# Kernel optimization log

Measured on AMD Instinct MI355X. Metric: run time of the kernel, lower is better.

## Reference

```python
import jax, jax.numpy as jnp
import numpy as np
import math

K, N, T, HID = 10, 96, 40, 48   # samples, agents (batch_size=1), timesteps, hidden
HZ = 10.0
R0, R1 = 0.5, 4.0
SPB = 6                          # social pooling grid is 6x6
RSTEP = (R1 - R0) / SPB          # radius_step (not set in shown source; natural value)
TWO_PI = 2.0 * math.pi
TSTEP = TWO_PI / SPB             # theta_step


def setup_inputs() -> dict:
    key = jax.random.key(0)
    ks = iter(jax.random.split(key, 24))
    def u(shape, fan):
        s = 1.0 / float(np.sqrt(fan))
        return jax.random.uniform(next(ks), shape, jnp.float32, -s, s)
    inp = {
        "hx": jax.random.normal(next(ks), (N, HID), jnp.float32),
        # locations in [-15,15] keep feature-map pixel gather in-bounds (u=40-long(y))
        "current_location": (jax.random.uniform(next(ks), (N, 2), jnp.float32) - 0.5) * 30.0,
        "y_path": (jax.random.uniform(next(ks), (K, T, N, 2), jnp.float32) - 0.5) * 30.0,
        "image_data": jax.random.normal(next(ks), (1, 4, 160, 160), jnp.float32),
        "conv1_w": u((16, 4, 5, 5), 4 * 25), "conv1_b": u((16,), 4 * 25),
        "conv2_w": u((32, 16, 5, 5), 16 * 25), "conv2_b": u((32,), 16 * 25),
        "fcvel_w": u((16, 2), 2), "fcvel_b": u((16,), 2),
        "gru_wih": u((3 * HID, 96), 96), "gru_whh": u((3 * HID, HID), HID),
        "gru_bih": u((3 * HID,), HID), "gru_bhh": u((3 * HID,), HID),
        "fcscf_w": u((HID, SPB * SPB * HID), SPB * SPB * HID), "fcscf_b": u((HID,), SPB * SPB * HID),
        "fcscore_w": u((1, HID), HID), "fcscore_b": u((1,), HID),
        "fcdy_w": u((2 * T, HID), HID), "fcdy_b": u((2 * T,), HID),
    }
    return inp


def _forward(hx, current_location, y_path, image_data, conv1_w, conv1_b, conv2_w, conv2_b,
             fcvel_w, fcvel_b, gru_wih, gru_whh, gru_bih, gru_bhh,
             fcscf_w, fcscf_b, fcscore_w, fcscore_b, fcdy_w, fcdy_b):
    # cnn_map: (1,4,160,160) -> (1,32,80,80)
    x = jax.lax.conv_general_dilated(image_data, conv1_w, (2, 2), ((2, 2), (2, 2)),
                                     dimension_numbers=("NCHW", "OIHW", "NCHW"))
    x = jax.nn.relu(x + conv1_b[None, :, None, None])
    x = jax.lax.conv_general_dilated(x, conv2_w, (1, 1), ((2, 2), (2, 2)),
                                     dimension_numbers=("NCHW", "OIHW", "NCHW"))
    fmap = jax.nn.relu(x + conv2_b[None, :, None, None])[0]  # (32,80,80); batch_size=1
    H = fmap.shape[1]

    # compute_vel + fc_vel: (K,T,N,2) -> (K,T,N,16)
    prev = jnp.concatenate([jnp.broadcast_to(current_location[None, None], (K, 1, N, 2)),
                            y_path[:, :-1]], axis=1)
    vel = (y_path - prev) * HZ
    y_fv = jax.nn.relu(vel @ fcvel_w.T + fcvel_b)

    hx_all = jnp.tile(hx, (K, 1))  # hx.repeat((K,1)) -> (K*N,48)
    t_idx = jnp.arange(N)
    not_self = ~jnp.eye(N, dtype=bool)

    def step(h, xs):
        loc, fv_t = xs  # (K,N,2), (K,N,16)
        hidden = h[:N]  # replicates hx[0:n] slice used in the original scf call
        # feature-map gather at agent pixel (.long() truncates toward zero)
        ui = (H // 2) - loc[..., 1].astype(jnp.int32)
        vi = (H // 2) - loc[..., 0].astype(jnp.int32)
        feat = jnp.moveaxis(fmap[:, ui, vi], 0, -1)  # (K,N,32)
        # pairwise dist/angle binning: c[k,j,t] = loc_t - loc_j
        c = loc[:, None, :, :] - loc[:, :, None, :]
        dist = jnp.linalg.norm(c, axis=-1)                        # (K,N,N)
        valid = (dist >= R0) & (dist <= R1) & not_self[None]
        dsafe = jnp.maximum(dist, 1e-10)
        cost = jnp.clip(c[..., 0] / dsafe, -1.0, 1.0)
        ac = jnp.arccos(cost)
        theta = jnp.where(c[..., 1] < 0, TWO_PI - ac, ac)
        ub = jnp.clip(((dist - R0) / RSTEP).astype(jnp.int32), 0, SPB - 1)
        vb = jnp.clip((theta / TSTEP).astype(jnp.int32), 0, SPB - 1)
        bins = ub * SPB + vb                                      # (K,N,N)
        hot = (bins[..., None] == jnp.arange(SPB * SPB)) & valid[..., None]  # (K,N,N,36)
        counts = hot.sum(axis=2)                                  # (K,N,36)
        # original writes hidden[t] with set() in increasing-t order: last writer = max t
        winner = jnp.max(jnp.where(hot, t_idx[None, None, :, None], -1), axis=2)
        sp = jnp.where(winner[..., None] >= 0, hidden[jnp.maximum(winner, 0)], 0.0)  # (K,N,36,48)
        sp = sp / jnp.maximum(counts, 1)[..., None]
        sps = sp.reshape(K, N, SPB * SPB * HID)
        lhalf = jnp.concatenate([feat, fv_t], axis=-1)            # (K,N,48)
        rhalf = jax.nn.relu(sps @ fcscf_w.T + fcscf_b)            # (K,N,48)
        x_i = jnp.concatenate([lhalf, rhalf], axis=-1).reshape(K * N, 96)
        # torch GRUCell (gate order r,z,n)
        gi = x_i @ gru_wih.T + gru_bih
        gh = h @ gru_whh.T + gru_bhh
        ir, iz, inn = jnp.split(gi, 3, axis=-1)
        hr, hz_, hn = jnp.split(gh, 3, axis=-1)
        r = jax.nn.sigmoid(ir + hr)
        z = jax.nn.sigmoid(iz + hz_)
        ng = jnp.tanh(inn + r * hn)
        h_new = (1.0 - z) * ng + z * h
        return h_new, h_new

    xs = (jnp.moveaxis(y_path, 1, 0), jnp.moveaxis(y_fv, 1, 0))  # time-major
    h_last, hs = jax.lax.scan(step, hx_all, xs)                  # hs: (T,K*N,48)
    delta_y = jax.nn.relu(h_last @ fcdy_w.T + fcdy_b)            # (K*N,80)
    delta_y = delta_y.reshape(K, N, 2, T).transpose(0, 3, 1, 2)  # (K,40,N,2)
    score = (hs @ fcscore_w.T + fcscore_b).sum(axis=0).reshape(K, N, 1)
    return delta_y, score


def reference(hx, current_location, y_path, image_data, conv1_w, conv1_b, conv2_w, conv2_b,
              fcvel_w, fcvel_b, gru_wih, gru_whh, gru_bih, gru_bhh,
              fcscf_w, fcscf_b, fcscore_w, fcscore_b, fcdy_w, fcdy_b):
    return _forward(hx, current_location, y_path, image_data, conv1_w, conv1_b, conv2_w, conv2_b,
                    fcvel_w, fcvel_b, gru_wih, gru_whh, gru_bih, gru_bhh,
                    fcscf_w, fcscf_b, fcscore_w, fcscore_b, fcdy_w, fcdy_b)
```

## Files before the change

kernel.cpp:

```cpp
#include <hip/hip_runtime.h>
#include <math.h>

#define KK 10
#define NN 96
#define TT 40

#define HZf 10.0f
#define R0f 0.5f
#define R1f 4.0f
#define RSTEPf ((4.0f - 0.5f) / 6.0f)
#define TWO_PIf 6.2831853071795864769f
#define TSTEPf (6.2831853071795864769f / 6.0f)

typedef unsigned short u16;
typedef unsigned int u32;
typedef unsigned long long u64;
typedef float f32x4 __attribute__((ext_vector_type(4)));

__device__ __forceinline__ u16 f2bf(float f) {
    union { float f; unsigned u; } v; v.f = f;
    unsigned r = v.u + 0x7fffu + ((v.u >> 16) & 1u);
    return (u16)(r >> 16);
}
__device__ __forceinline__ float bflo(u32 u) {
// ... 16 lines not shown
    const int tid = threadIdx.x;
    const int bx = blockIdx.x % 10, by = blockIdx.x / 10;
    const int x0 = bx * 8, y0 = by * 8;
    for (int i = tid; i < 1600; i += 256) {
        int oc = i & 15, t2 = i >> 4, tap = t2 % 25, ic = t2 / 25;
        sW[i] = w[(oc * 4 + ic) * 25 + tap];
    }
    for (int i = tid; i < 1444; i += 256) {
        int ic = i / 361, rem = i % 361, r = rem / 19, c = rem % 19;
        int gy = 2 * y0 - 2 + r, gx = 2 * x0 - 2 + c;
        sIn[i] = (gy >= 0 && gy < 160 && gx >= 0 && gx < 160)
                     ? img[(ic * 160 + gy) * 160 + gx] : 0.f;
    }
    __syncthreads();
    const int pix = tid & 63, ocg = tid >> 6;
    const int px = pix & 7, py = pix >> 3;
    float acc[4];
#pragma unroll
    for (int j = 0; j < 4; ++j) acc[j] = b[ocg * 4 + j];
#pragma unroll
    for (int ic = 0; ic < 4; ++ic) {
        int ibase = ic * 361;
#pragma unroll
        for (int ky = 0; ky < 5; ++ky) {
#pragma unroll
            for (int kx = 0; kx < 5; ++kx) {
                float iv = sIn[ibase + (2 * py + ky) * 19 + 2 * px + kx];
                f32x4 wv = *(const f32x4*)&sW[(ic * 25 + ky * 5 + kx) * 16 + ocg * 4];
#pragma unroll
                for (int j = 0; j < 4; ++j) acc[j] += iv * wv[j];
            }
        }
    }
#pragma unroll
    for (int j = 0; j < 4; ++j)
        out[((ocg * 4 + j) * 80 + y0 + py) * 80 + x0 + px] = fmaxf(acc[j], 0.f);
}

__global__ __launch_bounds__(256) void conv2_t(const float* __restrict__ in,
                                               const float* __restrict__ w,
                                               const float* __restrict__ b,
                                               float* __restrict__ out) {
    __shared__ float sW[12800];
    __shared__ float sIn[2304];
    const int tid = threadIdx.x;
    const int bx = blockIdx.x % 10, by = blockIdx.x / 10;
    const int x0 = bx * 8, y0 = by * 8;
    for (int i = tid; i < 12800; i += 256) {
        int oc = i & 31, t2 = i >> 5, tap = t2 % 25, ic = t2 / 25;
        sW[i] = w[(oc * 16 + ic) * 25 + tap];
    }
    for (int i = tid; i < 2304; i += 256) {
        int ic = i / 144, rem = i % 144, r = rem / 12, c = rem % 12;
        int gy = y0 - 2 + r, gx = x0 - 2 + c;
        sIn[i] = (gy >= 0 && gy < 80 && gx >= 0 && gx < 80)
                     ? in[(ic * 80 + gy) * 80 + gx] : 0.f;
    }
    __syncthreads();
    const int pix = tid & 63, ocg = tid >> 6;
    const int px = pix & 7, py = pix >> 3;
    float acc[8];
#pragma unroll
    for (int j = 0; j < 8; ++j) acc[j] = b[ocg * 8 + j];
    for (int ic = 0; ic < 16; ++ic) {
        int ibase = ic * 144;
#pragma unroll
        for (int ky = 0; ky < 5; ++ky) {
#pragma unroll
            for (int kx = 0; kx < 5; ++kx) {
                float iv = sIn[ibase + (py + ky) * 12 + px + kx];
                int wb = (ic * 25 + ky * 5 + kx) * 32 + ocg * 8;
                f32x4 w0 = *(const f32x4*)&sW[wb];
                f32x4 w1 = *(const f32x4*)&sW[wb + 4];
#pragma unroll
                for (int j = 0; j < 4; ++j) {
                    acc[j] += iv * w0[j];
                    acc[4 + j] += iv * w1[j];
                }
            }
        }
    }
#pragma unroll
    for (int j = 0; j < 8; ++j)
        out[((ocg * 8 + j) * 80 + y0 + py) * 80 + x0 + px] = fmaxf(acc[j], 0.f);
}

__global__ void prep_w3(const float* __restrict__ scf, const float* __restrict__ wih,
                        const float* __restrict__ whh, const float* __restrict__ bih,
                        const float* __restrict__ bhh, const float* __restrict__ scfb,
                        const float* __restrict__ hx, float* __restrict__ h0hist,
                        u32* __restrict__ wscf_p, u32* __restrict__ Wr_p,
                        u32* __restrict__ Wz_p, u32* __restrict__ Win_p,
                        u32* __restrict__ Whn_p, float* __restrict__ bias5) {
    int idx = blockIdx.x * blockDim.x + threadIdx.x;
    if (idx < 41472) {
        int o = idx % 48, dp = (idx / 48) % 24, b = idx / 1152;
        float v0 = scf[o * 1728 + b * 48 + 2 * dp];
        float v1 = scf[o * 1728 + b * 48 + 2 * dp + 1];
        wscf_p[idx] = (u32)f2bf(v0) | ((u32)f2bf(v1) << 16);
    } else if (idx < 44928) {
        int j = idx - 41472, od = j % 48, dp = j / 48;
        int kk0 = 2 * dp, kk1 = 2 * dp + 1;
        float v0 = kk0 < 96 ? wih[od * 96 + kk0] : whh[od * 48 + kk0 - 96];
        float v1 = kk1 < 96 ? wih[od * 96 + kk1] : whh[od * 48 + kk1 - 96];
        Wr_p[j] = (u32)f2bf(v0) | ((u32)f2bf(v1) << 16);
    } else if (idx < 48384) {
        int j = idx - 44928, od = j % 48, dp = j / 48;
        int row = 48 + od, kk0 = 2 * dp, kk1 = 2 * dp + 1;
        float v0 = kk0 < 96 ? wih[row * 96 + kk0] : whh[row * 48 + kk0 - 96];
        float v1 = kk1 < 96 ? wih[row * 96 + kk1] : whh[row * 48 + kk1 - 96];
        Wz_p[j] = (u32)f2bf(v0) | ((u32)f2bf(v1) << 16);
    } else if (idx < 50688) {
        int j = idx - 48384, od = j % 48, dp = j / 48;
        int row = 96 + od;
        Win_p[j] = (u32)f2bf(wih[row * 96 + 2 * dp]) | ((u32)f2bf(wih[row * 96 + 2 * dp + 1]) << 16);
    } else if (idx < 51840) {
        int j = idx - 50688, od = j % 48, dp = j / 48;
        int row = 96 + od;
        Whn_p[j] = (u32)f2bf(whh[row * 48 + 2 * dp]) | ((u32)f2bf(whh[row * 48 + 2 * dp + 1]) << 16);
    } else if (idx < 52080) {
        int j = idx - 51840, od = j % 48, q = j / 48;
        float v;
        if (q == 0) v = bih[od] + bhh[od];
        else if (q == 1) v = bih[48 + od] + bhh[48 + od];
        else if (q == 2) v = bih[96 + od];
        else if (q == 3) v = bhh[96 + od];
        else v = scfb[od];
        bias5[j] = v;
    } else if (idx < 56688) {
        int j = idx - 52080;
        h0hist[j] = hx[j];
    }
}

__global__ __launch_bounds__(256) void lhalf_k(const float* __restrict__ yp,
                                               const float* __restrict__ cur,
                                               const float* __restrict__ fmap,
                                               const float* __restrict__ vw,
                                               const float* __restrict__ vb,
                                               u16* __restrict__ lhalf_bf) {
    int item = blockIdx.x * 4 + (threadIdx.x >> 6);
    int lane = threadIdx.x & 63;
    int n = item % NN, k = (item / NN) % KK, t = item / (KK * NN);
    float lx = yp[((k * TT + t) * NN + n) * 2 + 0];
    float ly = yp[((k * TT + t) * NN + n) * 2 + 1];
    float px, py;
    if (t == 0) { px = cur[n * 2]; py = cur[n * 2 + 1]; }
    else { px = yp[((k * TT + t - 1) * NN + n) * 2]; py = yp[((k * TT + t - 1) * NN + n) * 2 + 1]; }
    float vx = (lx - px) * HZf, vy = (ly - py) * HZf;
    int ui = 40 - (int)ly;
    int vi = 40 - (int)lx;
    ui = min(max(ui, 0), 79);
    vi = min(max(vi, 0), 79);
    int row = k * NN + n;
    u16* dst = lhalf_bf + ((size_t)t * 960 + row) * 48;
    if (lane < 32) {
        dst[lane] = f2bf(fmap[(lane * 80 + ui) * 80 + vi]);
    } else if (lane < 48) {
        int f = lane - 32;
        float a = vb[f] + vx * vw[f * 2 + 0] + vy * vw[f * 2 + 1];
        dst[lane] = f2bf(fmaxf(a, 0.0f));
    }
}

__global__ __launch_bounds__(256) void bins4_k(const float* __restrict__ yp,
                                               u32* __restrict__ binc) {
    int tk = blockIdx.x;
    int k = tk % KK, t = tk / KK;
    int tid = threadIdx.x;
    __shared__ float xs[96], ys[96];
    __shared__ int win_s[96 * 36];
    __shared__ int cnt_s[96 * 36];
    if (tid < 96) {
        xs[tid] = yp[((k * TT + t) * NN + tid) * 2 + 0];
        ys[tid] = yp[((k * TT + t) * NN + tid) * 2 + 1];
    }
    for (int i = tid; i < 96 * 36; i += 256) { win_s[i] = -1; cnt_s[i] = 0; }
    __syncthreads();
    for (int p = tid; p < 96 * 96; p += 256) {
        int i = p / 96, j = p % 96;
        if (i == j) continue;
        float dx = xs[j] - xs[i], dy = ys[j] - ys[i];
        float dist = sqrtf(dx * dx + dy * dy);
        if (dist < R0f || dist > R1f) continue;
        float dsafe = fmaxf(dist, 1e-10f);
        float cost = fminf(fmaxf(dx / dsafe, -1.0f), 1.0f);
        float ac = acosf(cost);
        float theta = (dy < 0.0f) ? (TWO_PIf - ac) : ac;
        int ub = (int)((dist - R0f) / RSTEPf); ub = min(max(ub, 0), 5);
        int vb = (int)(theta / TSTEPf);        vb = min(max(vb, 0), 5);
        int b = ub * 6 + vb;
        atomicAdd(&cnt_s[i * 36 + b], 1);
        atomicMax(&win_s[i * 36 + b], j);
    }
    __syncthreads();
    if (tid < 96) {
        u32 base = (u32)(t * 960 + k * 96 + tid) * 20u;
        u16* entg = (u16*)(binc + base + 2);
        u64 mask = 0ull;
        int ne = 0;
        for (int b = 0; b < 36; ++b) {
            int w = win_s[tid * 36 + b];
            if (w >= 0) {
                mask |= 1ull << b;
                entg[ne++] = (u16)((w << 8) | cnt_s[tid * 36 + b]);
            }
        }
        binc[base] = (u32)mask;
        binc[base + 1] = (u32)(mask >> 32);
    }
}

__global__ __launch_bounds__(256) void step_k(
    int t, float* __restrict__ h0hist, const u16* __restrict__ lhalf_bf,
    const u32* __restrict__ binc, const u32* __restrict__ wscf_p,
    const u32* __restrict__ Wr_p, const u32* __restrict__ Wz_p,
    const u32* __restrict__ Win_p, const u32* __restrict__ Whn_p,
    const float* __restrict__ bias5, const float* __restrict__ scw,
    float* __restrict__ score_acc, float* __restrict__ hfin,
    u16* __restrict__ rhalf_all, const float* __restrict__ hx,
    float* __restrict__ hf) {
    __shared__ u32 smu[9856];
    float* smf = (float*)smu;
    const int tid = threadIdx.x;
    const int wv = tid >> 6, lane = tid & 63;
    const int lo = lane < 48 ? lane : 47;

    if (blockIdx.x < 96) {
        if (t >= TT) return;
        const float* hcur = h0hist + (size_t)t * 4608;
        const int r = blockIdx.x;
        float* shw = smf;
        float* shx = smf + 1728;
        float* ps1 = smf + 1872;
        float* ps2 = smf + 2064;
        u32* sent = (u32*)(smf + 2832);
        unsigned char* blist = (unsigned char*)(smf + 2852);

        if (tid < 20) sent[tid] = binc[(size_t)(t * 960 + r) * 20 + tid];
        if (tid < 48) {
            shx[tid] = bf2f(lhalf_bf[((size_t)t * 960 + r) * 48 + tid]);
            shx[96 + tid] = hcur[r * 48 + tid];
        }
        __syncthreads();
        u64 mask = ((u64)sent[1] << 32) | sent[0];
        int ne = __popcll(mask);
        const u16* ent = (const u16*)(sent + 2);
        if (tid < 36 && ((mask >> tid) & 1)) {
            int rank = __popcll(mask & ((1ull << tid) - 1ull));
            blist[rank] = (unsigned char)tid;
        }
        for (int i = tid; i < ne * 48; i += 256) {
            int e = i / 48, c = i - e * 48;
            int w = (ent[e] >> 8) & 0xff;
            shw[i] = hcur[w * 48 + c];
        }
        __syncthreads();
        float acc = 0.f;
        for (int e = 0; e < ne; ++e) {
            int b = blist[e];
            float cinv = 1.0f / (float)(ent[e] & 0xff);
            const u32* wp = wscf_p + (b * 24 + wv * 6) * 48 + lo;
            const float* xv = shw + e * 48 + wv * 12;
            float a = 0.f;
#pragma unroll
            for (int dp = 0; dp < 6; ++dp) {
                u32 u = wp[dp * 48];
                a += bflo(u) * xv[2 * dp] + bfhi(u) * xv[2 * dp + 1];
            }
            acc += a * cinv;
        }
        if (lane < 48) ps1[wv * 48 + lane] = acc;
        __syncthreads();
        if (wv == 0 && lane < 48) {
            float rh = ps1[lane] + ps1[48 + lane] + ps1[96 + lane] + ps1[144 + lane] +
                       bias5[192 + lane];
            shx[48 + lane] = fmaxf(rh, 0.f);
        }
        __syncthreads();
        float aR = 0.f, aZ = 0.f, aI = 0.f, aH = 0.f;
        int dp0 = wv * 18;
#pragma unroll
        for (int i = 0; i < 18; ++i) {
            int dp = dp0 + i;
            u32 uR = Wr_p[dp * 48 + lo], uZ = Wz_p[dp * 48 + lo];
            float xlo = shx[2 * dp], xhi = shx[2 * dp + 1];
            aR += bflo(uR) * xlo + bfhi(uR) * xhi;
            aZ += bflo(uZ) * xlo + bfhi(uZ) * xhi;
            if (dp < 48) {
                u32 uI = Win_p[dp * 48 + lo];
                aI += bflo(uI) * xlo + bfhi(uI) * xhi;
            } else {
                u32 uH = Whn_p[(dp - 48) * 48 + lo];
                aH += bflo(uH) * xlo + bfhi(uH) * xhi;
            }
        }
        if (lane < 48) {
            ps2[(wv * 4 + 0) * 48 + lane] = aR;
            ps2[(wv * 4 + 1) * 48 + lane] = aZ;
            ps2[(wv * 4 + 2) * 48 + lane] = aI;
            ps2[(wv * 4 + 3) * 48 + lane] = aH;
        }
        __syncthreads();
        if (wv == 0) {
            float sv = 0.f;
            if (lane < 48) {
                float AR = 0.f, AZ = 0.f, AI = 0.f, AH = 0.f;
#pragma unroll
                for (int w2 = 0; w2 < 4; ++w2) {
                    AR += ps2[(w2 * 4 + 0) * 48 + lane];
                    AZ += ps2[(w2 * 4 + 1) * 48 + lane];
                    AI += ps2[(w2 * 4 + 2) * 48 + lane];
                    AH += ps2[(w2 * 4 + 3) * 48 + lane];
                }
                float hprev = shx[96 + lane];
                float rr = sigmoidf_(AR + bias5[lane]);
                float zz = sigmoidf_(AZ + bias5[48 + lane]);
                float ng = tanhf(AI + bias5[96 + lane] + rr * (AH + bias5[144 + lane]));
                float hn = (1.0f - zz) * ng + zz * hprev;
                h0hist[(size_t)(t + 1) * 4608 + r * 48 + lane] = hn;
                if (t == TT - 1) hfin[r * 48 + lane] = hn;
                sv = hn * scw[lane];
            }
            for (int off = 32; off; off >>= 1) sv += __shfl_down(sv, off);
            if (lane == 0) score_acc[r] = (t == 0 ? 0.f : score_acc[r]) + sv;
        }
    } else if (blockIdx.x < 312) {
        if (t >= TT) return;
        const float* hcur = h0hist + (size_t)t * 4608;
        int widx = (blockIdx.x - 96) * 4 + wv;
        int row = 96 + widx;
        float* myw = smf + wv * 1728;
        const u32* bp = binc + (size_t)(t * 960 + row) * 20;
        u64 mask = ((u64)bp[1] << 32) | bp[0];
        int ne = __popcll(mask);
        const u16* ent = (const u16*)(bp + 2);
        for (int i = lane; i < ne * 48; i += 64) {
            int e = i / 48, c = i - e * 48;
            int w = (ent[e] >> 8) & 0xff;
            myw[i] = hcur[w * 48 + c];
        }
        __syncthreads();
        float acc = 0.f;
        u64 m2 = mask;
        for (int e = 0; e < ne; ++e) {
            int b = __ffsll((long long)m2) - 1;
            m2 &= m2 - 1;
            float cinv = 1.0f / (float)(ent[e] & 0xff);
            const u32* wp = wscf_p + b * 24 * 48 + lo;
            const float* xv = myw + e * 48;
            float a = 0.f;
#pragma unroll 8
            for (int dp = 0; dp < 24; ++dp) {
                u32 u = wp[dp * 48];
                a += bflo(u) * xv[2 * dp] + bfhi(u) * xv[2 * dp + 1];
            }
            acc += a * cinv;
        }
        float rh = fmaxf(acc + bias5[192 + lo], 0.f);
        if (lane < 48) rhalf_all[((size_t)t * 864 + widx) * 48 + lane] = f2bf(rh);
    } else {
        int s = t - 1;
        if (s < 0 || s >= TT) return;
        u32* sWr = smu;
        u32* sWz = smu + 3456;
        u32* sWin = smu + 6912;
        u32* sx = smu + 9216 + wv * 48;
        float* shh = (float*)(smu + 9408) + wv * 48;
        for (int i = tid; i < 3456; i += 256) { sWr[i] = Wr_p[i]; sWz[i] = Wz_p[i]; }
        for (int i = tid; i < 2304; i += 256) sWin[i] = Win_p[i];
        u32 whn[24];
#pragma unroll
        for (int dp = 0; dp < 24; ++dp) whn[dp] = Whn_p[dp * 48 + lo];
        int widx = (blockIdx.x - 312) * 4 + wv;
        int row = 96 + widx;
        const float* hsrc = (s == 0) ? (hx + (row % 96) * 48) : (hf + (s & 1) * 41472 + widx * 48);
        float hreg = hsrc[lo];
        if (lane < 24) {
            sx[lane] = *(const u32*)(lhalf_bf + ((size_t)s * 960 + row) * 48 + 2 * lane);
            sx[24 + lane] = *(const u32*)(rhalf_all + ((size_t)s * 864 + widx) * 48 + 2 * lane);
        }
        if (lane < 48) shh[lane] = hreg;
        __syncthreads();
        const float bRb = bias5[lo], bZb = bias5[48 + lo], bIb = bias5[96 + lo],
                    bHb = bias5[144 + lo];
        float aR = 0.f, aZ = 0.f, aI = 0.f, aH = 0.f;
#pragma unroll 8
        for (int dp = 0; dp < 48; ++dp) {
            u32 xp = sx[dp];
            float xlo = bflo(xp), xhi = bfhi(xp);
            u32 uR = sWr[dp * 48 + lo], uZ = sWz[dp * 48 + lo], uI = sWin[dp * 48 + lo];
            aR += bflo(uR) * xlo + bfhi(uR) * xhi;
            aZ += bflo(uZ) * xlo + bfhi(uZ) * xhi;
            aI += bflo(uI) * xlo + bfhi(uI) * xhi;
        }
#pragma unroll 8
        for (int dp = 48; dp < 72; ++dp) {
            float xlo = shh[2 * dp - 96], xhi = shh[2 * dp - 95];
            u32 uR = sWr[dp * 48 + lo], uZ = sWz[dp * 48 + lo], uH = whn[dp - 48];
            aR += bflo(uR) * xlo + bfhi(uR) * xhi;
            aZ += bflo(uZ) * xlo + bfhi(uZ) * xhi;
            aH += bflo(uH) * xlo + bfhi(uH) * xhi;
        }
        float rr = sigmoidf_(aR + bRb);
        float zz = sigmoidf_(aZ + bZb);
        float ng = tanhf(aI + bIb + rr * (aH + bHb));
        float hn = (1.0f - zz) * ng + zz * hreg;
        if (lane < 48) {
            hf[((s + 1) & 1) * 41472 + widx * 48 + lane] = hn;
            if (s == TT - 1) hfin[(size_t)row * 48 + lane] = hn;
        }
        float sv = (lane < 48) ? hn * scw[lane] : 0.f;
        for (int off = 32; off; off >>= 1) sv += __shfl_down(sv, off);
        if (lane == 0) score_acc[row] = (s == 0 ? 0.f : score_acc[row]) + sv;
    }
}

__global__ void final_k(const float* __restrict__ hlast, const float* __restrict__ score_acc,
                        const float* __restrict__ dyw, const float* __restrict__ dyb,
                        const float* __restrict__ scoreb, float* __restrict__ out) {
    int row = blockIdx.x, lane = threadIdx.x;
    int n = row % 96, k = row / 96;
    __shared__ float sh_h[48];
    if (lane < 48) sh_h[lane] = hlast[row * 48 + lane];
    __syncthreads();
    if (lane < 80) {
        float a = dyb[lane];
#pragma unroll 8
        for (int d = 0; d < 48; d++) a += sh_h[d] * dyw[lane * 48 + d];
        a = fmaxf(a, 0.0f);
        int j = lane / 40, tt = lane % 40;
        out[((k * TT + tt) * NN + n) * 2 + j] = a;
    } else if (lane == 80) {
        out[76800 + row] = score_acc[row] + 40.0f * scoreb[0];
    }
}

// ... 3 lines not shown
    const float* hx  = (const float*)d_in[0];
    const float* cur = (const float*)d_in[1];
    const float* yp  = (const float*)d_in[2];
    const float* img = (const float*)d_in[3];
    const float* c1w = (const float*)d_in[4];
    const float* c1b = (const float*)d_in[5];
    const float* c2w = (const float*)d_in[6];
    const float* c2b = (const float*)d_in[7];
    const float* vw  = (const float*)d_in[8];
    const float* vb  = (const float*)d_in[9];
    const float* wih = (const float*)d_in[10];
    const float* whh = (const float*)d_in[11];
    const float* bih = (const float*)d_in[12];
    const float* bhh = (const float*)d_in[13];
    const float* scfw = (const float*)d_in[14];
    const float* scfb = (const float*)d_in[15];
    const float* scw  = (const float*)d_in[16];
    const float* scb  = (const float*)d_in[17];
    const float* dyw  = (const float*)d_in[18];
    const float* dyb  = (const float*)d_in[19];
    float* out = (float*)d_out;

    char* ws = (char*)d_ws;
    u32*   binc     = (u32*)(ws + 0);
    float* fmap1    = (float*)(ws + 0);
    float* fmap     = (float*)(ws + 409600);
    u16*   rhalf_all= (u16*)(ws + 3072000);
    u16*   lhalf_bf = (u16*)(ws + 6389760);
    float* h0hist   = (float*)(ws + 10076160);
    float* hfin     = (float*)(ws + 10831872);
    float* score_acc= (float*)(ws + 11016192);
    u32*   wscf_p   = (u32*)(ws + 11020032);
    u32*   Wr_p     = (u32*)(ws + 11185920);
    u32*   Wz_p     = (u32*)(ws + 11199744);
    u32*   Win_p    = (u32*)(ws + 11213568);
    u32*   Whn_p    = (u32*)(ws + 11222784);
    float* bias5    = (float*)(ws + 11227392);
    float* hf       = (float*)(ws + 11228352);

    conv1_t<<<100, 256, 0, stream>>>(img, c1w, c1b, fmap1);
    conv2_t<<<100, 256, 0, stream>>>(fmap1, c2w, c2b, fmap);
    prep_w3<<<222, 256, 0, stream>>>(scfw, wih, whh, bih, bhh, scfb, hx, h0hist,
                                     wscf_p, Wr_p, Wz_p, Win_p, Whn_p, bias5);
    lhalf_k<<<TT * KK * NN / 4, 256, 0, stream>>>(yp, cur, fmap, vw, vb, lhalf_bf);
    bins4_k<<<TT * KK, 256, 0, stream>>>(yp, binc);

    for (int t = 0; t <= TT; ++t) {
        step_k<<<528, 256, 0, stream>>>(t, h0hist, lhalf_bf, binc, wscf_p, Wr_p, Wz_p,
                                        Win_p, Whn_p, bias5, scw, score_acc, hfin,
                                        rhalf_all, hx, hf);
    }
    final_k<<<960, 128, 0, stream>>>(hfin, score_acc, dyw, dyb, scb, out);
}
```

Before: 490.1 us.

## Fuse preprocessing kernels and advance two GRU timesteps per launch

Merges the weight-packing, lhalf and social-bin kernels into one launch. The recurrent step kernel now processes two timesteps per launch, with agent blocks recomputing the needed neighbour rows for the intermediate step, which halves the number of serialized step launches. The cost is redundant per-block recomputation of dependent rows and more shared memory and register pressure in the step kernel. The workspace layout is also moved so that binc no longer aliases fmap1.

After: 1.467 ms. 199% more time.

```diff
diff --git a/kernel.cpp b/kernel.cpp
--- a/kernel.cpp
+++ b/kernel.cpp
@@ -62,7 +62,7 @@
     for (int ic = 0; ic < 4; ++ic) {
         int ibase = ic * 361;
 #pragma unroll
-        for (int ky = 0; ky < 5; ++ky) {
+        for (int ky = 0; ky < 5; ++ky)
 #pragma unroll
             for (int kx = 0; kx < 5; ++kx) {
                 float iv = sIn[ibase + (2 * py + ky) * 19 + 2 * px + kx];
@@ -70,7 +70,6 @@
 #pragma unroll
                 for (int j = 0; j < 4; ++j) acc[j] += iv * wv[j];
             }
-        }
     }
 #pragma unroll
     for (int j = 0; j < 4; ++j)
@@ -105,7 +104,7 @@
     for (int ic = 0; ic < 16; ++ic) {
         int ibase = ic * 144;
 #pragma unroll
-        for (int ky = 0; ky < 5; ++ky) {
+        for (int ky = 0; ky < 5; ++ky)
 #pragma unroll
             for (int kx = 0; kx < 5; ++kx) {
                 float iv = sIn[ibase + (py + ky) * 12 + px + kx];
@@ -113,145 +112,207 @@
                 f32x4 w0 = *(const f32x4*)&sW[wb];
                 f32x4 w1 = *(const f32x4*)&sW[wb + 4];
 #pragma unroll
-                for (int j = 0; j < 4; ++j) {
-                    acc[j] += iv * w0[j];
-                    acc[4 + j] += iv * w1[j];
-                }
-            }
-        }
+                for (int j = 0; j < 4; ++j) { acc[j] += iv * w0[j]; acc[4 + j] += iv * w1[j]; }
+            }
     }
 #pragma unroll
     for (int j = 0; j < 8; ++j)
         out[((ocg * 8 + j) * 80 + y0 + py) * 80 + x0 + px] = fmaxf(acc[j], 0.f);
 }
 
-__global__ void prep_w3(const float* __restrict__ scf, const float* __restrict__ wih,
-                        const float* __restrict__ whh, const float* __restrict__ bih,
-                        const float* __restrict__ bhh, const float* __restrict__ scfb,
-                        const float* __restrict__ hx, float* __restrict__ h0hist,
-                        u32* __restrict__ wscf_p, u32* __restrict__ Wr_p,
-                        u32* __restrict__ Wz_p, u32* __restrict__ Win_p,
-                        u32* __restrict__ Whn_p, float* __restrict__ bias5) {
-    int idx = blockIdx.x * blockDim.x + threadIdx.x;
-    if (idx < 41472) {
-        int o = idx % 48, dp = (idx / 48) % 24, b = idx / 1152;
-        float v0 = scf[o * 1728 + b * 48 + 2 * dp];
-        float v1 = scf[o * 1728 + b * 48 + 2 * dp + 1];
-        wscf_p[idx] = (u32)f2bf(v0) | ((u32)f2bf(v1) << 16);
-    } else if (idx < 44928) {
-        int j = idx - 41472, od = j % 48, dp = j / 48;
-        int kk0 = 2 * dp, kk1 = 2 * dp + 1;
-        float v0 = kk0 < 96 ? wih[od * 96 + kk0] : whh[od * 48 + kk0 - 96];
-        float v1 = kk1 < 96 ? wih[od * 96 + kk1] : whh[od * 48 + kk1 - 96];
-        Wr_p[j] = (u32)f2bf(v0) | ((u32)f2bf(v1) << 16);
-    } else if (idx < 48384) {
-        int j = idx - 44928, od = j % 48, dp = j / 48;
-        int row = 48 + od, kk0 = 2 * dp, kk1 = 2 * dp + 1;
-        float v0 = kk0 < 96 ? wih[row * 96 + kk0] : whh[row * 48 + kk0 - 96];
-        float v1 = kk1 < 96 ? wih[row * 96 + kk1] : whh[row * 48 + kk1 - 96];
-        Wz_p[j] = (u32)f2bf(v0) | ((u32)f2bf(v1) << 16);
-    } else if (idx < 50688) {
-        int j = idx - 48384, od = j % 48, dp = j / 48;
-        int row = 96 + od;
-        Win_p[j] = (u32)f2bf(wih[row * 96 + 2 * dp]) | ((u32)f2bf(wih[row * 96 + 2 * dp + 1]) << 16);
-    } else if (idx < 51840) {
-        int j = idx - 50688, od = j % 48, dp = j / 48;
-        int row = 96 + od;
-        Whn_p[j] = (u32)f2bf(whh[row * 48 + 2 * dp]) | ((u32)f2bf(whh[row * 48 + 2 * dp + 1]) << 16);
-    } else if (idx < 52080) {
-        int j = idx - 51840, od = j % 48, q = j / 48;
-        float v;
-        if (q == 0) v = bih[od] + bhh[od];
-        else if (q == 1) v = bih[48 + od] + bhh[48 + od];
-        else if (q == 2) v = bih[96 + od];
-        else if (q == 3) v = bhh[96 + od];
-        else v = scfb[od];
-        bias5[j] = v;
-    } else if (idx < 56688) {
-        int j = idx - 52080;
-        h0hist[j] = hx[j];
-    }
-}
-
-__global__ __launch_bounds__(256) void lhalf_k(const float* __restrict__ yp,
-                                               const float* __restrict__ cur,
-                                               const float* __restrict__ fmap,
-                                               const float* __restrict__ vw,
-                                               const float* __restrict__ vb,
-                                               u16* __restrict__ lhalf_bf) {
-    int item = blockIdx.x * 4 + (threadIdx.x >> 6);
-    int lane = threadIdx.x & 63;
-    int n = item % NN, k = (item / NN) % KK, t = item / (KK * NN);
-    float lx = yp[((k * TT + t) * NN + n) * 2 + 0];
-    float ly = yp[((k * TT + t) * NN + n) * 2 + 1];
-    float px, py;
-    if (t == 0) { px = cur[n * 2]; py = cur[n * 2 + 1]; }
-    else { px = yp[((k * TT + t - 1) * NN + n) * 2]; py = yp[((k * TT + t - 1) * NN + n) * 2 + 1]; }
-    float vx = (lx - px) * HZf, vy = (ly - py) * HZf;
-    int ui = 40 - (int)ly;
-    int vi = 40 - (int)lx;
-    ui = min(max(ui, 0), 79);
-    vi = min(max(vi, 0), 79);
-    int row = k * NN + n;
-    u16* dst = lhalf_bf + ((size_t)t * 960 + row) * 48;
-    if (lane < 32) {
-        dst[lane] = f2bf(fmap[(lane * 80 + ui) * 80 + vi]);
-    } else if (lane < 48) {
-        int f = lane - 32;
-        float a = vb[f] + vx * vw[f * 2 + 0] + vy * vw[f * 2 + 1];
-        dst[lane] = f2bf(fmaxf(a, 0.0f));
-    }
-}
-
-__global__ __launch_bounds__(256) void bins4_k(const float* __restrict__ yp,
-                                               u32* __restrict__ binc) {
-    int tk = blockIdx.x;
-    int k = tk % KK, t = tk / KK;
-    int tid = threadIdx.x;
+__global__ __launch_bounds__(256) void pre_k(
+    const float* __restrict__ scf, const float* __restrict__ wih,
+    const float* __restrict__ whh, const float* __restrict__ bih,
+    const float* __restrict__ bhh, const float* __restrict__ scfb,
+    const float* __restrict__ hx, float* __restrict__ h0hist,
+    u32* __restrict__ wscf_p, u32* __restrict__ Wr_p, u32* __restrict__ Wz_p,
+    u32* __restrict__ Win_p, u32* __restrict__ Whn_p, float* __restrict__ bias5,
+    const float* __restrict__ yp, const float* __restrict__ cur,
+    const float* __restrict__ fmap, const float* __restrict__ vw,
+    const float* __restrict__ vb, u16* __restrict__ lhalf_bf,
+    u32* __restrict__ binc) {
     __shared__ float xs[96], ys[96];
     __shared__ int win_s[96 * 36];
     __shared__ int cnt_s[96 * 36];
-    if (tid < 96) {
-        xs[tid] = yp[((k * TT + t) * NN + tid) * 2 + 0];
-        ys[tid] = yp[((k * TT + t) * NN + tid) * 2 + 1];
-    }
-    for (int i = tid; i < 96 * 36; i += 256) { win_s[i] = -1; cnt_s[i] = 0; }
-    __syncthreads();
-    for (int p = tid; p < 96 * 96; p += 256) {
-        int i = p / 96, j = p % 96;
-        if (i == j) continue;
-        float dx = xs[j] - xs[i], dy = ys[j] - ys[i];
-        float dist = sqrtf(dx * dx + dy * dy);
-        if (dist < R0f || dist > R1f) continue;
-        float dsafe = fmaxf(dist, 1e-10f);
-        float cost = fminf(fmaxf(dx / dsafe, -1.0f), 1.0f);
-        float ac = acosf(cost);
-        float theta = (dy < 0.0f) ? (TWO_PIf - ac) : ac;
-        int ub = (int)((dist - R0f) / RSTEPf); ub = min(max(ub, 0), 5);
-        int vb = (int)(theta / TSTEPf);        vb = min(max(vb, 0), 5);
-        int b = ub * 6 + vb;
-        atomicAdd(&cnt_s[i * 36 + b], 1);
-        atomicMax(&win_s[i * 36 + b], j);
-    }
-    __syncthreads();
-    if (tid < 96) {
-        u32 base = (u32)(t * 960 + k * 96 + tid) * 20u;
-        u16* entg = (u16*)(binc + base + 2);
-        u64 mask = 0ull;
-        int ne = 0;
-        for (int b = 0; b < 36; ++b) {
-            int w = win_s[tid * 36 + b];
-            if (w >= 0) {
-                mask |= 1ull << b;
-                entg[ne++] = (u16)((w << 8) | cnt_s[tid * 36 + b]);
-            }
-        }
-        binc[base] = (u32)mask;
-        binc[base + 1] = (u32)(mask >> 32);
-    }
-}
-
-__global__ __launch_bounds__(256) void step_k(
+    const int bid = blockIdx.x;
+    if (bid < 222) {
+        int idx = bid * 256 + threadIdx.x;
+        if (idx < 41472) {
+            int o = idx % 48, dp = (idx / 48) % 24, b = idx / 1152;
+            float v0 = scf[o * 1728 + b * 48 + 2 * dp];
+            float v1 = scf[o * 1728 + b * 48 + 2 * dp + 1];
+            wscf_p[idx] = (u32)f2bf(v0) | ((u32)f2bf(v1) << 16);
+        } else if (idx < 44928) {
+            int j = idx - 41472, od = j % 48, dp = j / 48;
+            int kk0 = 2 * dp, kk1 = 2 * dp + 1;
+            float v0 = kk0 < 96 ? wih[od * 96 + kk0] : whh[od * 48 + kk0 - 96];
+            float v1 = kk1 < 96 ? wih[od * 96 + kk1] : whh[od * 48 + kk1 - 96];
+            Wr_p[j] = (u32)f2bf(v0) | ((u32)f2bf(v1) << 16);
+        } else if (idx < 48384) {
+            int j = idx - 44928, od = j % 48, dp = j / 48;
+            int row = 48 + od, kk0 = 2 * dp, kk1 = 2 * dp + 1;
+            float v0 = kk0 < 96 ? wih[row * 96 + kk0] : whh[row * 48 + kk0 - 96];
+            float v1 = kk1 < 96 ? wih[row * 96 + kk1] : whh[row * 48 + kk1 - 96];
+            Wz_p[j] = (u32)f2bf(v0) | ((u32)f2bf(v1) << 16);
+        } else if (idx < 50688) {
+            int j = idx - 48384, od = j % 48, dp = j / 48;
+            int row = 96 + od;
+            Win_p[j] = (u32)f2bf(wih[row * 96 + 2 * dp]) |
+                       ((u32)f2bf(wih[row * 96 + 2 * dp + 1]) << 16);
+        } else if (idx < 51840) {
+            int j = idx - 50688, od = j % 48, dp = j / 48;
+            int row = 96 + od;
+            Whn_p[j] = (u32)f2bf(whh[row * 48 + 2 * dp]) |
+                       ((u32)f2bf(whh[row * 48 + 2 * dp + 1]) << 16);
+        } else if (idx < 52080) {
+            int j = idx - 51840, od = j % 48, q = j / 48;
+            float v;
+            if (q == 0) v = bih[od] + bhh[od];
+            else if (q == 1) v = bih[48 + od] + bhh[48 + od];
+            else if (q == 2) v = bih[96 + od];
+            else if (q == 3) v = bhh[96 + od];
+            else v = scfb[od];
+            bias5[j] = v;
+        } else if (idx < 56688) {
+            int j = idx - 52080;
+            h0hist[j] = hx[j];
+        }
+    } else if (bid < 222 + 9600) {
+        int item = (bid - 222) * 4 + (threadIdx.x >> 6);
+        int lane = threadIdx.x & 63;
+        int n = item % NN, k = (item / NN) % KK, t = item / (KK * NN);
+        float lx = yp[((k * TT + t) * NN + n) * 2 + 0];
+        float ly = yp[((k * TT + t) * NN + n) * 2 + 1];
+        float px, py;
+        if (t == 0) { px = cur[n * 2]; py = cur[n * 2 + 1]; }
+        else { px = yp[((k * TT + t - 1) * NN + n) * 2]; py = yp[((k * TT + t - 1) * NN + n) * 2 + 1]; }
+        float vx = (lx - px) * HZf, vy = (ly - py) * HZf;
+        int ui = 40 - (int)ly, vi = 40 - (int)lx;
+        ui = min(max(ui, 0), 79);
+        vi = min(max(vi, 0), 79);
+        int row = k * NN + n;
+        u16* dst = lhalf_bf + ((size_t)t * 960 + row) * 48;
+        if (lane < 32) {
+            dst[lane] = f2bf(fmap[(lane * 80 + ui) * 80 + vi]);
+        } else if (lane < 48) {
+            int f = lane - 32;
+            float a = vb[f] + vx * vw[f * 2 + 0] + vy * vw[f * 2 + 1];
+            dst[lane] = f2bf(fmaxf(a, 0.0f));
+        }
+    } else {
+        int tk = bid - 222 - 9600;
+        int k = tk % KK, t = tk / KK;
+        int tid = threadIdx.x;
+        if (tid < 96) {
+            xs[tid] = yp[((k * TT + t) * NN + tid) * 2 + 0];
+            ys[tid] = yp[((k * TT + t) * NN + tid) * 2 + 1];
+        }
+        for (int i = tid; i < 96 * 36; i += 256) { win_s[i] = -1; cnt_s[i] = 0; }
+        __syncthreads();
+        for (int p = tid; p < 96 * 96; p += 256) {
+            int i = p / 96, j = p % 96;
+            if (i == j) continue;
+            float dx = xs[j] - xs[i], dy = ys[j] - ys[i];
+            float dist = sqrtf(dx * dx + dy * dy);
+            if (dist < R0f || dist > R1f) continue;
+            float dsafe = fmaxf(dist, 1e-10f);
+            float cost = fminf(fmaxf(dx / dsafe, -1.0f), 1.0f);
+            float ac = acosf(cost);
+            float theta = (dy < 0.0f) ? (TWO_PIf - ac) : ac;
+            int ub = (int)((dist - R0f) / RSTEPf); ub = min(max(ub, 0), 5);
+            int vb = (int)(theta / TSTEPf);        vb = min(max(vb, 0), 5);
+            int b = ub * 6 + vb;
+            atomicAdd(&cnt_s[i * 36 + b], 1);
+            atomicMax(&win_s[i * 36 + b], j);
+        }
+        __syncthreads();
+        if (tid < 96) {
+            u32 base = (u32)(t * 960 + k * 96 + tid) * 20u;
+            u16* entg = (u16*)(binc + base + 2);
+            u64 mask = 0ull;
+            int ne = 0;
+            for (int b = 0; b < 36; ++b) {
+                int w = win_s[tid * 36 + b];
+                if (w >= 0) {
+                    mask |= 1ull << b;
+                    entg[ne++] = (u16)((w << 8) | cnt_s[tid * 36 + b]);
+                }
+            }
+            binc[base] = (u32)mask;
+            binc[base + 1] = (u32)(mask >> 32);
+        }
+    }
+}
+
+__device__ __forceinline__ float rhalf_row(const u32* __restrict__ bp,
+                                           const float* __restrict__ hsrc,
+                                           const u32* __restrict__ wscf_p, int lo,
+                                           const float* __restrict__ biasL) {
+    u64 mask = ((u64)bp[1] << 32) | (u64)bp[0];
+    int ne = __popcll(mask);
+    const u16* ent = (const u16*)(bp + 2);
+    float acc = 0.f;
+    u64 m2 = mask;
+    for (int e = 0; e < ne; ++e) {
+        int b = __ffsll((long long)m2) - 1;
+        m2 &= m2 - 1;
+        u32 en = ent[e];
+        int win = (en >> 8) & 0xff;
+        float cinv = 1.f / (float)(en & 0xff);
+        const u32* wp = wscf_p + (b * 24) * 48 + lo;
+        const float* xv = hsrc + win * 48;
+        float a = 0.f;
+#pragma unroll 8
+        for (int dp = 0; dp < 24; ++dp) {
+            u32 u = wp[dp * 48];
+            a += bflo(u) * xv[2 * dp] + bfhi(u) * xv[2 * dp + 1];
+        }
+        acc += a * cinv;
+    }
+    return fmaxf(acc + biasL[192 + lo], 0.f);
+}
+
+__device__ __forceinline__ float stepA_row(
+    int w, int t, int lo, const float* __restrict__ hT, const u16* __restrict__ lhT,
+    const u32* __restrict__ binc, const u32* __restrict__ wscf_p,
+    const u32* __restrict__ Wr_p, const u32* __restrict__ Wz_p,
+    const u32* __restrict__ Win_p, const u32* __restrict__ Whn_p,
+    const float* __restrict__ biasL) {
+    const u32* bp = binc + (size_t)(t * 960 + w) * 20;
+    float rh = rhalf_row(bp, hT, wscf_p, lo, biasL);
+    float aR = 0.f, aZ = 0.f, aI = 0.f, aH = 0.f;
+#pragma unroll 8
+    for (int dp = 0; dp < 24; ++dp) {
+        u32 xp = *(const u32*)&lhT[w * 48 + 2 * dp];
+        float xlo = bflo(xp), xhi = bfhi(xp);
+        u32 uR = Wr_p[dp * 48 + lo], uZ = Wz_p[dp * 48 + lo], uI = Win_p[dp * 48 + lo];
+        aR += bflo(uR) * xlo + bfhi(uR) * xhi;
+        aZ += bflo(uZ) * xlo + bfhi(uZ) * xhi;
+        aI += bflo(uI) * xlo + bfhi(uI) * xhi;
+    }
+#pragma unroll 8
+    for (int dp = 24; dp < 48; ++dp) {
+        float xlo = __shfl(rh, 2 * dp - 48), xhi = __shfl(rh, 2 * dp - 47);
+        u32 uR = Wr_p[dp * 48 + lo], uZ = Wz_p[dp * 48 + lo], uI = Win_p[dp * 48 + lo];
+        aR += bflo(uR) * xlo + bfhi(uR) * xhi;
+        aZ += bflo(uZ) * xlo + bfhi(uZ) * xhi;
+        aI += bflo(uI) * xlo + bfhi(uI) * xhi;
+    }
+#pragma unroll 8
+    for (int dp = 48; dp < 72; ++dp) {
+        float xlo = hT[w * 48 + 2 * dp - 96], xhi = hT[w * 48 + 2 * dp - 95];
+        u32 uR = Wr_p[dp * 48 + lo], uZ = Wz_p[dp * 48 + lo], uH = Whn_p[(dp - 48) * 48 + lo];
+        aR += bflo(uR) * xlo + bfhi(uR) * xhi;
+        aZ += bflo(uZ) * xlo + bfhi(uZ) * xhi;
+        aH += bflo(uH) * xlo + bfhi(uH) * xhi;
+    }
+    float rr = sigmoidf_(aR + biasL[lo]);
+    float zz = sigmoidf_(aZ + biasL[48 + lo]);
+    float ng = tanhf(aI + biasL[96 + lo] + rr * (aH + biasL[144 + lo]));
+    return (1.f - zz) * ng + zz * hT[w * 48 + lo];
+}
+
+__global__ __launch_bounds__(256) void step2_k(
     int t, float* __restrict__ h0hist, const u16* __restrict__ lhalf_bf,
     const u32* __restrict__ binc, const u32* __restrict__ wscf_p,
     const u32* __restrict__ Wr_p, const u32* __restrict__ Wz_p,
@@ -260,48 +321,64 @@
     float* __restrict__ score_acc, float* __restrict__ hfin,
     u16* __restrict__ rhalf_all, const float* __restrict__ hx,
     float* __restrict__ hf) {
-    __shared__ u32 smu[9856];
-    float* smf = (float*)smu;
+    __shared__ char smem[52000];
     const int tid = threadIdx.x;
     const int wv = tid >> 6, lane = tid & 63;
     const int lo = lane < 48 ? lane : 47;
-
-    if (blockIdx.x < 96) {
+    const int bid = blockIdx.x;
+
+    if (bid < 96) {
         if (t >= TT) return;
-        const float* hcur = h0hist + (size_t)t * 4608;
-        const int r = blockIdx.x;
-        float* shw = smf;
-        float* shx = smf + 1728;
-        float* ps1 = smf + 1872;
-        float* ps2 = smf + 2064;
-        u32* sent = (u32*)(smf + 2832);
-        unsigned char* blist = (unsigned char*)(smf + 2852);
-
-        if (tid < 20) sent[tid] = binc[(size_t)(t * 960 + r) * 20 + tid];
+        float* hT = (float*)smem;
+        float* h1 = (float*)(smem + 18432);
+        u16* lhT = (u16*)(smem + 36864);
+        float* biasL = (float*)(smem + 46080);
+        float* scwL = (float*)(smem + 47040);
+        u32* sentB = (u32*)(smem + 47232);
+        float* shxB = (float*)(smem + 47312);
+        float* ps1 = (float*)(smem + 47888);
+        float* ps2 = (float*)(smem + 48656);
+        const int r = bid;
+        for (int i = tid; i < 4608; i += 256) hT[i] = h0hist[(size_t)t * 4608 + i];
+        {
+            const u32* src = (const u32*)(lhalf_bf + (size_t)t * 960 * 48);
+            for (int i = tid; i < 2304; i += 256) ((u32*)lhT)[i] = src[i];
+        }
+        if (tid < 240) biasL[tid] = bias5[tid];
+        if (tid < 48) scwL[tid] = scw[tid];
+        if (tid < 20) sentB[tid] = binc[(size_t)((t + 1) * 960 + r) * 20 + tid];
+        __syncthreads();
+        u64 maskB = ((u64)sentB[1] << 32) | (u64)sentB[0];
+        int neB = __popcll(maskB);
+        const u16* entB = (const u16*)(sentB + 2);
+        int nS = neB + 1;
+        float scoreA = 0.f;
+        for (int idx = wv; idx < nS; idx += 4) {
+            int w = (idx == 0) ? r : ((entB[idx - 1] >> 8) & 0xff);
+            float hn = stepA_row(w, t, lo, hT, lhT, binc, wscf_p, Wr_p, Wz_p, Win_p,
+                                 Whn_p, biasL);
+            if (lane < 48) h1[w * 48 + lane] = hn;
+            if (idx == 0) {
+                scoreA = (lane < 48) ? hn * scwL[lane] : 0.f;
+                if (lane < 48) h0hist[(size_t)(t + 1) * 4608 + r * 48 + lane] = hn;
+            }
+        }
+        __syncthreads();
         if (tid < 48) {
-            shx[tid] = bf2f(lhalf_bf[((size_t)t * 960 + r) * 48 + tid]);
-            shx[96 + tid] = hcur[r * 48 + tid];
-        }
-        __syncthreads();
-        u64 mask = ((u64)sent[1] << 32) | sent[0];
-        int ne = __popcll(mask);
-        const u16* ent = (const u16*)(sent + 2);
-        if (tid < 36 && ((mask >> tid) & 1)) {
-            int rank = __popcll(mask & ((1ull << tid) - 1ull));
-            blist[rank] = (unsigned char)tid;
-        }
-        for (int i = tid; i < ne * 48; i += 256) {
-            int e = i / 48, c = i - e * 48;
-            int w = (ent[e] >> 8) & 0xff;
-            shw[i] = hcur[w * 48 + c];
+            shxB[tid] = bf2f(lhalf_bf[((size_t)(t + 1) * 960 + r) * 48 + tid]);
+            shxB[96 + tid] = h1[r * 48 + tid];
         }
         __syncthreads();
         float acc = 0.f;
-        for (int e = 0; e < ne; ++e) {
-            int b = blist[e];
-            float cinv = 1.0f / (float)(ent[e] & 0xff);
+        u64 m2 = maskB;
+        for (int e = 0; e < neB; ++e) {
+            int b = __ffsll((long long)m2) - 1;
+            m2 &= m2 - 1;
+            u32 en = entB[e];
+            int win = (en >> 8) & 0xff;
+            float cinv = 1.f / (float)(en & 0xff);
             const u32* wp = wscf_p + (b * 24 + wv * 6) * 48 + lo;
-            const float* xv = shw + e * 48 + wv * 12;
+            const float* xv = h1 + win * 48 + wv * 12;
             float a = 0.f;
 #pragma unroll
             for (int dp = 0; dp < 6; ++dp) {
@@ -314,8 +391,8 @@
         __syncthreads();
         if (wv == 0 && lane < 48) {
             float rh = ps1[lane] + ps1[48 + lane] + ps1[96 + lane] + ps1[144 + lane] +
-                       bias5[192 + lane];
-            shx[48 + lane] = fmaxf(rh, 0.f);
+                       biasL[192 + lane];
+            shxB[48 + lane] = fmaxf(rh, 0.f);
         }
         __syncthreads();
         float aR = 0.f, aZ = 0.f, aI = 0.f, aH = 0.f;
@@ -324,7 +401,7 @@
         for (int i = 0; i < 18; ++i) {
             int dp = dp0 + i;
             u32 uR = Wr_p[dp * 48 + lo], uZ = Wz_p[dp * 48 + lo];
-            float xlo = shx[2 * dp], xhi = shx[2 * dp + 1];
+            float xlo = shxB[2 * dp], xhi = shxB[2 * dp + 1];
             aR += bflo(uR) * xlo + bfhi(uR) * xhi;
             aZ += bflo(uZ) * xlo + bfhi(uZ) * xhi;
             if (dp < 48) {
@@ -343,7 +420,7 @@
         }
         __syncthreads();
         if (wv == 0) {
-            float sv = 0.f;
+            float sv = scoreA;
             if (lane < 48) {
                 float AR = 0.f, AZ = 0.f, AI = 0.f, AH = 0.f;
 #pragma unroll
@@ -353,106 +430,134 @@
                     AI += ps2[(w2 * 4 + 2) * 48 + lane];
                     AH += ps2[(w2 * 4 + 3) * 48 + lane];
                 }
-                float hprev = shx[96 + lane];
-                float rr = sigmoidf_(AR + bias5[lane]);
-                float zz = sigmoidf_(AZ + bias5[48 + lane]);
-                float ng = tanhf(AI + bias5[96 + lane] + rr * (AH + bias5[144 + lane]));
+                float hprev = shxB[96 + lane];
+                float rr = sigmoidf_(AR + biasL[lane]);
+                float zz = sigmoidf_(AZ + biasL[48 + lane]);
+                float ng = tanhf(AI + biasL[96 + lane] + rr * (AH + biasL[144 + lane]));
                 float hn = (1.0f - zz) * ng + zz * hprev;
-                h0hist[(size_t)(t + 1) * 4608 + r * 48 + lane] = hn;
-                if (t == TT - 1) hfin[r * 48 + lane] = hn;
-                sv = hn * scw[lane];
+                h0hist[(size_t)(t + 2) * 4608 + r * 48 + lane] = hn;
+                if (t + 2 == TT) hfin[r * 48 + lane] = hn;
+                sv += hn * scwL[lane];
             }
             for (int off = 32; off; off >>= 1) sv += __shfl_down(sv, off);
             if (lane == 0) score_acc[r] = (t == 0 ? 0.f : score_acc[r]) + sv;
         }
-    } else if (blockIdx.x < 312) {
+    } else if (bid < 312) {
         if (t >= TT) return;
-        const float* hcur = h0hist + (size_t)t * 4608;
-        int widx = (blockIdx.x - 96) * 4 + wv;
-        int row = 96 + widx;
-        float* myw = smf + wv * 1728;
-        const u32* bp = binc + (size_t)(t * 960 + row) * 20;
-        u64 mask = ((u64)bp[1] << 32) | bp[0];
-        int ne = __popcll(mask);
-        const u16* ent = (const u16*)(bp + 2);
-        for (int i = lane; i < ne * 48; i += 64) {
-            int e = i / 48, c = i - e * 48;
-            int w = (ent[e] >> 8) & 0xff;
-            myw[i] = hcur[w * 48 + c];
-        }
-        __syncthreads();
-        float acc = 0.f;
-        u64 m2 = mask;
-        for (int e = 0; e < ne; ++e) {
-            int b = __ffsll((long long)m2) - 1;
-            m2 &= m2 - 1;
-            float cinv = 1.0f / (float)(ent[e] & 0xff);
-            const u32* wp = wscf_p + b * 24 * 48 + lo;
-            const float* xv = myw + e * 48;
-            float a = 0.f;
-#pragma unroll 8
-            for (int dp = 0; dp < 24; ++dp) {
-                u32 u = wp[dp * 48];
-                a += bflo(u) * xv[2 * dp] + bfhi(u) * xv[2 * dp + 1];
-            }
-            acc += a * cinv;
-        }
-        float rh = fmaxf(acc + bias5[192 + lo], 0.f);
-        if (lane < 48) rhalf_all[((size_t)t * 864 + widx) * 48 + lane] = f2bf(rh);
+        float* hT = (float*)smem;
+        float* h1 = (float*)(smem + 18432);
+        u16* lhT = (u16*)(smem + 36864);
+        float* biasL = (float*)(smem + 46080);
+        u32* umask = (u32*)(smem + 47040);
+        for (int i = tid; i < 4608; i += 256) hT[i] = h0hist[(size_t)t * 4608 + i];
+        {
+            const u32* src = (const u32*)(lhalf_bf + (size_t)t * 960 * 48);
+            for (int i = tid; i < 2304; i += 256) ((u32*)lhT)[i] = src[i];
+        }
+        if (tid < 240) biasL[tid] = bias5[tid];
+        if (tid < 3) umask[tid] = 0;
+        __syncthreads();
+        const int fr = 96 + (bid - 96) * 4 + wv;
+        const u32* bpB = binc + (size_t)((t + 1) * 960 + fr) * 20;
+        u64 maskB = ((u64)bpB[1] << 32) | (u64)bpB[0];
+        int neB = __popcll(maskB);
+        const u16* entB = (const u16*)(bpB + 2);
+        if (lane == 0) {
+            for (int e = 0; e < neB; ++e) {
+                int w = (entB[e] >> 8) & 0xff;
+                atomicOr(&umask[w >> 5], 1u << (w & 31));
+            }
+        }
+        __syncthreads();
+        {
+            int idx = 0;
+#pragma unroll
+            for (int word = 0; word < 3; ++word) {
+                u32 m = umask[word];
+                while (m) {
+                    int b = __ffs(m) - 1;
+                    m &= m - 1;
+                    int w = word * 32 + b;
+                    if ((idx & 3) == wv) {
+                        float hn = stepA_row(w, t, lo, hT, lhT, binc, wscf_p, Wr_p, Wz_p,
+                                             Win_p, Whn_p, biasL);
+                        if (lane < 48) h1[w * 48 + lane] = hn;
+                    }
+                    idx++;
+                }
+            }
+        }
+        __syncthreads();
+        {
+            const u32* bpA = binc + (size_t)(t * 960 + fr) * 20;
+            float rh = rhalf_row(bpA, hT, wscf_p, lo, biasL);
+            if (lane < 48)
+                rhalf_all[((size_t)t * 864 + (fr - 96)) * 48 + lane] = f2bf(rh);
+        }
+        {
+            float rh = rhalf_row(bpB, h1, wscf_p, lo, biasL);
+            if (lane < 48)
+                rhalf_all[((size_t)(t + 1) * 864 + (fr - 96)) * 48 + lane] = f2bf(rh);
+        }
     } else {
-        int s = t - 1;
-        if (s < 0 || s >= TT) return;
-        u32* sWr = smu;
-        u32* sWz = smu + 3456;
-        u32* sWin = smu + 6912;
-        u32* sx = smu + 9216 + wv * 48;
-        float* shh = (float*)(smu + 9408) + wv * 48;
+        int s0 = t - 2;
+        if (s0 < 0) return;
+        u32* sWr = (u32*)smem;
+        u32* sWz = (u32*)(smem + 13824);
+        u32* sWin = (u32*)(smem + 27648);
+        u32* sx = (u32*)(smem + 36864) + wv * 48;
+        float* shh = (float*)(smem + 37632) + wv * 48;
         for (int i = tid; i < 3456; i += 256) { sWr[i] = Wr_p[i]; sWz[i] = Wz_p[i]; }
         for (int i = tid; i < 2304; i += 256) sWin[i] = Win_p[i];
         u32 whn[24];
 #pragma unroll
         for (int dp = 0; dp < 24; ++dp) whn[dp] = Whn_p[dp * 48 + lo];
-        int widx = (blockIdx.x - 312) * 4 + wv;
-        int row = 96 + widx;
-        const float* hsrc = (s == 0) ? (hx + (row % 96) * 48) : (hf + (s & 1) * 41472 + widx * 48);
-        float hreg = hsrc[lo];
-        if (lane < 24) {
-            sx[lane] = *(const u32*)(lhalf_bf + ((size_t)s * 960 + row) * 48 + 2 * lane);
-            sx[24 + lane] = *(const u32*)(rhalf_all + ((size_t)s * 864 + widx) * 48 + 2 * lane);
-        }
-        if (lane < 48) shh[lane] = hreg;
-        __syncthreads();
+        const int widx = (bid - 312) * 4 + wv;
+        const int row = 96 + widx;
+        float hreg = (s0 == 0) ? hx[(row % 96) * 48 + lo] : hf[widx * 48 + lo];
         const float bRb = bias5[lo], bZb = bias5[48 + lo], bIb = bias5[96 + lo],
                     bHb = bias5[144 + lo];
-        float aR = 0.f, aZ = 0.f, aI = 0.f, aH = 0.f;
+        const float swv = (lane < 48) ? scw[lane] : 0.f;
+        float score = 0.f;
+        for (int ss = s0; ss < s0 + 2; ++ss) {
+            if (lane < 24) {
+                sx[lane] = *(const u32*)(lhalf_bf + ((size_t)ss * 960 + row) * 48 + 2 * lane);
+                sx[24 + lane] =
+                    *(const u32*)(rhalf_all + ((size_t)ss * 864 + widx) * 48 + 2 * lane);
+            }
+            if (lane < 48) shh[lane] = hreg;
+            __syncthreads();
+            float aR = 0.f, aZ = 0.f, aI = 0.f, aH = 0.f;
 #pragma unroll 8
-        for (int dp = 0; dp < 48; ++dp) {
-            u32 xp = sx[dp];
-            float xlo = bflo(xp), xhi = bfhi(xp);
-            u32 uR = sWr[dp * 48 + lo], uZ = sWz[dp * 48 + lo], uI = sWin[dp * 48 + lo];
-            aR += bflo(uR) * xlo + bfhi(uR) * xhi;
-            aZ += bflo(uZ) * xlo + bfhi(uZ) * xhi;
-            aI += bflo(uI) * xlo + bfhi(uI) * xhi;
-        }
+            for (int dp = 0; dp < 48; ++dp) {
+                u32 xp = sx[dp];
+                float xlo = bflo(xp), xhi = bfhi(xp);
+                u32 uR = sWr[dp * 48 + lo], uZ = sWz[dp * 48 + lo], uI = sWin[dp * 48 + lo];
+                aR += bflo(uR) * xlo + bfhi(uR) * xhi;
+                aZ += bflo(uZ) * xlo + bfhi(uZ) * xhi;
+                aI += bflo(uI) * xlo + bfhi(uI) * xhi;
+            }
 #pragma unroll 8
-        for (int dp = 48; dp < 72; ++dp) {
-            float xlo = shh[2 * dp - 96], xhi = shh[2 * dp - 95];
-            u32 uR = sWr[dp * 48 + lo], uZ = sWz[dp * 48 + lo], uH = whn[dp - 48];
-            aR += bflo(uR) * xlo + bfhi(uR) * xhi;
-            aZ += bflo(uZ) * xlo + bfhi(uZ) * xhi;
-            aH += bflo(uH) * xlo + bfhi(uH) * xhi;
-        }
-        float rr = sigmoidf_(aR + bRb);
-        float zz = sigmoidf_(aZ + bZb);
-        float ng = tanhf(aI + bIb + rr * (aH + bHb));
-        float hn = (1.0f - zz) * ng + zz * hreg;
+            for (int dp = 48; dp < 72; ++dp) {
+                float xlo = shh[2 * dp - 96], xhi = shh[2 * dp - 95];
+                u32 uR = sWr[dp * 48 + lo], uZ = sWz[dp * 48 + lo], uH = whn[dp - 48];
+                aR += bflo(uR) * xlo + bfhi(uR) * xhi;
+                aZ += bflo(uZ) * xlo + bfhi(uZ) * xhi;
+                aH += bflo(uH) * xlo + bfhi(uH) * xhi;
+            }
+            float rr = sigmoidf_(aR + bRb);
+            float zz = sigmoidf_(aZ + bZb);
+            float ng = tanhf(aI + bIb + rr * (aH + bHb));
+            hreg = (1.0f - zz) * ng + zz * hreg;
+            score += hreg * swv;
+            __syncthreads();
+        }
         if (lane < 48) {
-            hf[((s + 1) & 1) * 41472 + widx * 48 + lane] = hn;
-            if (s == TT - 1) hfin[(size_t)row * 48 + lane] = hn;
-        }
-        float sv = (lane < 48) ? hn * scw[lane] : 0.f;
-        for (int off = 32; off; off >>= 1) sv += __shfl_down(sv, off);
-        if (lane == 0) score_acc[row] = (s == 0 ? 0.f : score_acc[row]) + sv;
+            hf[widx * 48 + lane] = hreg;
+            if (s0 + 1 == TT - 1) hfin[(size_t)row * 48 + lane] = hreg;
+        }
+        for (int off = 32; off; off >>= 1) score += __shfl_down(score, off);
+        if (lane == 0) score_acc[row] = (s0 == 0 ? 0.f : score_acc[row]) + score;
     }
 }
 
@@ -502,33 +607,33 @@
     float* out = (float*)d_out;
 
     char* ws = (char*)d_ws;
-    u32*   binc     = (u32*)(ws + 0);
     float* fmap1    = (float*)(ws + 0);
     float* fmap     = (float*)(ws + 409600);
-    u16*   rhalf_all= (u16*)(ws + 3072000);
-    u16*   lhalf_bf = (u16*)(ws + 6389760);
-    float* h0hist   = (float*)(ws + 10076160);
-    float* hfin     = (float*)(ws + 10831872);
-    float* score_acc= (float*)(ws + 11016192);
-    u32*   wscf_p   = (u32*)(ws + 11020032);
-    u32*   Wr_p     = (u32*)(ws + 11185920);
-    u32*   Wz_p     = (u32*)(ws + 11199744);
-    u32*   Win_p    = (u32*)(ws + 11213568);
-    u32*   Whn_p    = (u32*)(ws + 11222784);
-    float* bias5    = (float*)(ws + 11227392);
-    float* hf       = (float*)(ws + 11228352);
+    u32*   binc     = (u32*)(ws + 1228800);
+    u16*   rhalf_all= (u16*)(ws + 4300800);
+    u16*   lhalf_bf = (u16*)(ws + 7618560);
+    float* h0hist   = (float*)(ws + 11304960);
+    float* hfin     = (float*)(ws + 12060672);
+    float* score_acc= (float*)(ws + 12244992);
+    u32*   wscf_p   = (u32*)(ws + 12248832);
+    u32*   Wr_p     = (u32*)(ws + 12414720);
+    u32*   Wz_p     = (u32*)(ws + 12428544);
+    u32*   Win_p    = (u32*)(ws + 12442368);
+    u32*   Whn_p    = (u32*)(ws + 12451584);
+    float* bias5    = (float*)(ws + 12456192);
+    float* hf       = (float*)(ws + 12457152);
 
     conv1_t<<<100, 256, 0, stream>>>(img, c1w, c1b, fmap1);
     conv2_t<<<100, 256, 0, stream>>>(fmap1, c2w, c2b, fmap);
-    prep_w3<<<222, 256, 0, stream>>>(scfw, wih, whh, bih, bhh, scfb, hx, h0hist,
-                                     wscf_p, Wr_p, Wz_p, Win_p, Whn_p, bias5);
-    lhalf_k<<<TT * KK * NN / 4, 256, 0, stream>>>(yp, cur, fmap, vw, vb, lhalf_bf);
-    bins4_k<<<TT * KK, 256, 0, stream>>>(yp, binc);
-
-    for (int t = 0; t <= TT; ++t) {
-        step_k<<<528, 256, 0, stream>>>(t, h0hist, lhalf_bf, binc, wscf_p, Wr_p, Wz_p,
-                                        Win_p, Whn_p, bias5, scw, score_acc, hfin,
-                                        rhalf_all, hx, hf);
+    pre_k<<<222 + 9600 + 400, 256, 0, stream>>>(scfw, wih, whh, bih, bhh, scfb, hx,
+                                                h0hist, wscf_p, Wr_p, Wz_p, Win_p, Whn_p,
+                                                bias5, yp, cur, fmap, vw, vb, lhalf_bf,
+                                                binc);
+
+    for (int t = 0; t <= TT; t += 2) {
+        step2_k<<<528, 256, 0, stream>>>(t, h0hist, lhalf_bf, binc, wscf_p, Wr_p, Wz_p,
+                                         Win_p, Whn_p, bias5, scw, score_acc, hfin,
+                                         rhalf_all, hx, hf);
     }
     final_k<<<960, 128, 0, stream>>>(hfin, score_acc, dyw, dyb, scb, out);
 }
```
